# Optimization experiments

Measured on AMD Instinct MI355X. Metric: run time of the kernel, lower is better.

## Reference

```python
import jax, jax.numpy as jnp
import numpy as np

KS = (16, 16, 16)  # k per layer

def _knn_idx(pts, k):
    # pts: (P, C). Exclude self (knn_graph default loop=False).
    P = pts.shape[0]
    sq = jnp.sum(pts * pts, axis=1)
    d2 = sq[:, None] + sq[None, :] - 2.0 * (pts @ pts.T)  # (P, P)
    d2 = d2.at[jnp.arange(P), jnp.arange(P)].set(jnp.inf)
    _, idx = jax.lax.top_k(-d2, k)  # (P, k) nearest neighbors
    return idx

def _edge_conv(h, idx, W, b):
    # h: (P, C); idx: (P, k); W: (2C, Cout)
    hi = h[:, None, :]                      # (P, 1, C)
    hj = h[idx]                             # (P, k, C) gather
    msg = jnp.concatenate([jnp.broadcast_to(hi, hj.shape), hj - hi], axis=-1)
    m = msg @ W + b                         # (P, k, Cout)
    return jnp.max(m, axis=1)               # max aggregation -> (P, Cout)

def setup_inputs() -> dict:
    key = jax.random.key(0)
    ks = jax.random.split(key, 12)
    B, N, d = 2, 4096, 3
    chans = [d, 64, 128, 256]
    inp = {"x": jax.random.normal(ks[0], (B, N, d), dtype=jnp.float32)}
    for i in range(3):
        cin, cout = chans[i], chans[i + 1]
        s = 1.0 / np.sqrt(2 * cin)
        inp[f"W{i+1}"] = jax.random.uniform(ks[1 + 2 * i], (2 * cin, cout), jnp.float32, -s, s)
        inp[f"b{i+1}"] = jax.random.uniform(ks[2 + 2 * i], (cout,), jnp.float32, -s, s)
    s1 = 1.0 / np.sqrt(256.0)
    inp["fW1"] = jax.random.uniform(ks[7], (256, 128), jnp.float32, -s1, s1)
    inp["fb1"] = jax.random.uniform(ks[8], (128,), jnp.float32, -s1, s1)
    s2 = 1.0 / np.sqrt(128.0)
    inp["fW2"] = jax.random.uniform(ks[9], (128, 1), jnp.float32, -s2, s2)
    inp["fb2"] = jax.random.uniform(ks[10], (1,), jnp.float32, -s2, s2)
    return inp

def reference(x, W1, b1, W2, b2, W3, b3, fW1, fb1, fW2, fb2):
    B, N, _ = x.shape
    h = x.reshape(B * N, -1)  # KNN spans flattened batch (batch=None in source)
    for (W, b, k) in ((W1, b1, KS[0]), (W2, b2, KS[1]), (W3, b3, KS[2])):
        idx = _knn_idx(h, k)
        h = jax.nn.relu(_edge_conv(h, idx, W, b))
    out = jax.nn.relu(h @ fW1 + fb1) @ fW2 + fb2  # (P, 1)
    return out.reshape(B, N, 1)
```

## Files before the change

### kernel.cpp

```cpp
#include <hip/hip_runtime.h>
#include <hip/hip_bf16.h>

#define PTS 8192
#define NSPLIT 8

__device__ __forceinline__ void top_init(float (&bd)[16], int (&bi)[16]) {
#pragma unroll
  for (int t = 0; t < 16; ++t) { bd[t] = 3e38f; bi[t] = 0; }
}

__device__ __forceinline__ void top_insert(float (&bd)[16], int (&bi)[16], float d, int j) {
  if (d < bd[15]) {
#pragma unroll
    for (int t = 15; t >= 0; --t) {
      bool c  = d < bd[t];
      bool cp = (t > 0) ? (d < bd[t - 1]) : false;
      float nd = cp ? bd[t - 1] : d;
      int   ni = cp ? bi[t - 1] : j;
      if (c) { bd[t] = nd; bi[t] = ni; }
    }
  }
}

__global__ void sqnorm_kernel(const float* __restrict__ h, float* __restrict__ sq, int C) {
  int i = blockIdx.x * 256 + threadIdx.x;
  if (i >= PTS) return;
  const float* r = h + (size_t)i * C;
  float s = 0.f;
  if ((C & 3) == 0) {
    for (int k = 0; k < C; k += 4) {
      float4 v = *(const float4*)(r + k);
      s += v.x * v.x + v.y * v.y + v.z * v.z + v.w * v.w;
    }
  } else {
    for (int k = 0; k < C; ++k) s += r[k] * r[k];
  }
  sq[i] = s;
}

template <int C>
__global__ __launch_bounds__(256) void knn_kernel(const float* __restrict__ H,
                                                  const float* __restrict__ sq,
                                                  float* __restrict__ pd,
                                                  int* __restrict__ pi) {
  constexpr int KC = (C < 32) ? C : 32;
  constexpr int NC = C / KC;
  constexpr int TT = (PTS / NSPLIT) / 64;
  constexpr int N  = TT * NC;

  __shared__ __align__(128) float AsF[C * 64];
  __shared__ __align__(128) float S[2 * 32 * 64];

  const int tid  = threadIdx.x;
  const int b    = blockIdx.x;
  const int sy   = b & 7;
  const int sx   = b >> 3;
  const int row0 = sx * 64;
  const int cb   = sy * (PTS / NSPLIT);
  const int tx = tid & 15, ty = tid >> 4;
  const int r_ = tid & 63, g_ = tid >> 6;

  if constexpr (C >= 32) {
    const int r = tid >> 2, q = tid & 3;
#pragma unroll
    for (int j = 0; j < C / 16; ++j) {
      float4 v = *(const float4*)(H + (size_t)(row0 + r) * C + (q + j * 4) * 4);
      float vv[4] = {v.x, v.y, v.z, v.w};
#pragma unroll
      for (int e = 0; e < 4; ++e)
        AsF[((q + j * 4) * 4 + e) * 64 + r] = vv[e];
    }
  } else {
    if (tid < 16 * C) {
      float4 v = *(const float4*)(H + (size_t)row0 * C + tid * 4);
      float vv[4] = {v.x, v.y, v.z, v.w};
#pragma unroll
      for (int e = 0; e < 4; ++e) {
        int gi = tid * 4 + e;
        AsF[(gi % C) * 64 + gi / C] = vv[e];
      }
    }
  }

  float sqr[4];
#pragma unroll
  for (int u = 0; u < 4; ++u) sqr[u] = sq[row0 + ty * 4 + u];

  float bd[16]; int bi[16];
  top_init(bd, bi);

  float4 st0 = make_float4(0.f, 0.f, 0.f, 0.f);
  float4 st1 = make_float4(0.f, 0.f, 0.f, 0.f);
  auto stage_load = [&](int n1) {
    if constexpr (C >= 32) {
      const int c = tid >> 2, qj = tid & 3;
      const float* src = H + (size_t)(cb + (n1 / NC) * 64 + c) * C + (n1 % NC) * KC + qj * 8;
      st0 = *(const float4*)(src);
      st1 = *(const float4*)(src + 4);
    } else {
      if (tid < 16 * C) st0 = *(const float4*)(H + (size_t)(cb + n1 * 64) * C + tid * 4);
    }
  };
  auto stage_write = [&](int n1) {
    float* B = S + (n1 & 1) * 2048;
    if constexpr (C >= 32) {
      const int c = tid >> 2, qj = tid & 3;
      float v0[4] = {st0.x, st0.y, st0.z, st0.w};
      float v1[4] = {st1.x, st1.y, st1.z, st1.w};
#pragma unroll
      for (int e = 0; e < 4; ++e) {
        B[(qj * 8 + e) * 64 + c]     = v0[e];
        B[(qj * 8 + 4 + e) * 64 + c] = v1[e];
      }
    } else {
      if (tid < 16 * C) {
        float v0[4] = {st0.x, st0.y, st0.z, st0.w};
#pragma unroll
        for (int e = 0; e < 4; ++e) {
          int gi = tid * 4 + e;
          B[(gi % C) * 64 + gi / C] = v0[e];
        }
      }
    }
  };

  stage_load(0);
  stage_write(0);
  __syncthreads();

  float acc[4][4] = {};
  for (int n = 0; n < N; ++n) {
    if (n + 1 < N) stage_load(n + 1);
    const float* Bh = S + (n & 1) * 2048;
    const int kc = (n % NC) * KC;
#pragma unroll
    for (int k = 0; k < KC; ++k) {
      float4 a4 = *(const float4*)(AsF + (kc + k) * 64 + ty * 4);
      float4 b4 = *(const float4*)(Bh + k * 64 + tx * 4);
      float a[4]  = {a4.x, a4.y, a4.z, a4.w};
      float bb[4] = {b4.x, b4.y, b4.z, b4.w};
#pragma unroll
      for (int u = 0; u < 4; ++u)
#pragma unroll
        for (int v = 0; v < 4; ++v)
          acc[u][v] += a[u] * bb[v];
    }
    if ((n % NC) == NC - 1) {
      const int ct = (n / NC) * 64;
      float sqc[4];
#pragma unroll
      for (int v = 0; v < 4; ++v) sqc[v] = sq[cb + ct + tx * 4 + v];
      __syncthreads();
#pragma unroll
      for (int u = 0; u < 4; ++u) {
        int row = ty * 4 + u;
        int gr  = row0 + row;
        float dv[4];
#pragma unroll
        for (int v = 0; v < 4; ++v) {
          float d2 = sqr[u] + sqc[v] - 2.f * acc[u][v];
          if (gr == cb + ct + tx * 4 + v) d2 = 3e38f;
          dv[v] = d2;
          acc[u][v] = 0.f;
        }
        *(float4*)(S + row * 64 + ((tx * 4) ^ ((row & 7) << 2))) =
            make_float4(dv[0], dv[1], dv[2], dv[3]);
      }
      __syncthreads();
      const int cbase = cb + ct;
      const int swr = (r_ & 7) << 2;
      unsigned mask = 0;
#pragma unroll
      for (int q = 0; q < 16; ++q) {
        int cc = g_ * 16 + ((q + r_) & 15);
        float d = S[r_ * 64 + (cc ^ swr)];
        if (d < bd[15]) mask |= (1u << q);
      }
      while (__ballot(mask != 0)) {
        if (mask) {
          int q = __ffs(mask) - 1;
          mask &= mask - 1;
          int cc = g_ * 16 + ((q + r_) & 15);
          float d = S[r_ * 64 + (cc ^ swr)];
          top_insert(bd, bi, d, cbase + cc);
        }
      }
      __syncthreads();
    }
    if (n + 1 < N) {
      stage_write(n + 1);
      __syncthreads();
    }
  }

  if (g_ == 1 || g_ == 3) {
    float* base = S + (g_ == 3 ? 2048 : 0) + r_ * 32;
#pragma unroll
    for (int t = 0; t < 16; ++t) {
      int s = (t + r_) & 15;
      base[s] = bd[t];
      ((int*)base)[16 + s] = bi[t];
    }
  }
  __syncthreads();
  if (g_ == 0 || g_ == 2) {
    const float* base = S + (g_ == 2 ? 2048 : 0) + r_ * 32;
    for (int t = 0; t < 16; ++t) {
      int s = (t + r_) & 15;
      float d = base[s];
      if (d >= bd[15]) break;
      top_insert(bd, bi, d, ((const int*)base)[16 + s]);
    }
  }
  __syncthreads();
  if (g_ == 2) {
    float* base = S + r_ * 32;
#pragma unroll
    for (int t = 0; t < 16; ++t) {
      int s = (t + r_) & 15;
      base[s] = bd[t];
      ((int*)base)[16 + s] = bi[t];
    }
  }
  __syncthreads();
  if (g_ == 0) {
    const float* base = S + r_ * 32;
    for (int t = 0; t < 16; ++t) {
      int s = (t + r_) & 15;
      float d = base[s];
      if (d >= bd[15]) break;
      top_insert(bd, bi, d, ((const int*)base)[16 + s]);
    }
    size_t basep = ((size_t)(row0 + r_) * NSPLIT + sy) * 16;
#pragma unroll
    for (int t = 0; t < 16; ++t) { pd[basep + t] = bd[t]; pi[basep + t] = bi[t]; }
  }
}

__global__ void knn_merge_kernel(const float* __restrict__ pd, const int* __restrict__ pi,
                                 int* __restrict__ idx) {
  int i = blockIdx.x * 256 + threadIdx.x;
  if (i >= PTS) return;
  float bd[16]; int bi[16];
  top_init(bd, bi);
  const float* d  = pd + (size_t)i * (NSPLIT * 16);
  const int*   ii = pi + (size_t)i * (NSPLIT * 16);
  for (int L = 0; L < NSPLIT; ++L) {
    for (int t = 0; t < 16; ++t) {
      float dv = d[L * 16 + t];
      if (dv >= bd[15]) break;
      top_insert(bd, bi, dv, ii[L * 16 + t]);
    }
  }
#pragma unroll
  for (int t = 0; t < 16; ++t) idx[(size_t)i * 16 + t] = bi[t];
}

__global__ __launch_bounds__(256) void gemm_fg_kernel(const float* __restrict__ A,
                                                      const float* __restrict__ Wt,
                                                      const float* __restrict__ Wb,
                                                      const float* __restrict__ bias,
                                                      float* __restrict__ F, float* __restrict__ G,
                                                      int K, int N) {
  __shared__ float As[16][68];
  __shared__ float Bs[16][68];
  const int tid  = threadIdx.x;
  const int row0 = blockIdx.x * 64, col0 = blockIdx.y * 64;
  const float* B = (blockIdx.z == 0) ? Wt : Wb;
  float* O       = (blockIdx.z == 0) ? F  : G;
  const int tx = tid & 15, ty = tid >> 4;
  float acc[4][4] = {};
  for (int k0 = 0; k0 < K; k0 += 16) {
    __syncthreads();
#pragma unroll
    for (int l = 0; l < 4; ++l) {
      int rr = (tid >> 4) + l * 16, kk = tid & 15;
      As[kk][rr] = (k0 + kk < K) ? A[(size_t)(row0 + rr) * K + k0 + kk] : 0.f;
      int cc = tid & 63, k2 = (tid >> 6) + l * 4;
      Bs[k2][cc] = (k0 + k2 < K) ? B[(size_t)(k0 + k2) * N + col0 + cc] : 0.f;
    }
    __syncthreads();
#pragma unroll
    for (int k = 0; k < 16; ++k) {
      float4 a4 = *(const float4*)&As[k][ty * 4];
      float4 b4 = *(const float4*)&Bs[k][tx * 4];
      float a[4] = {a4.x, a4.y, a4.z, a4.w};
      float b[4] = {b4.x, b4.y, b4.z, b4.w};
#pragma unroll
      for (int u = 0; u < 4; ++u)
#pragma unroll
        for (int v = 0; v < 4; ++v)
          acc[u][v] += a[u] * b[v];
    }
  }
  float bv[4] = {0.f, 0.f, 0.f, 0.f};
  if (blockIdx.z == 0) {
#pragma unroll
    for (int v = 0; v < 4; ++v) bv[v] = bias[col0 + tx * 4 + v];
  }
#pragma unroll
  for (int u = 0; u < 4; ++u)
#pragma unroll
    for (int v = 0; v < 4; ++v)
      O[(size_t)(row0 + ty * 4 + u) * N + col0 + tx * 4 + v] = acc[u][v] + bv[v];
}

__global__ void gather_max_kernel(const float* __restrict__ F, const float* __restrict__ G,
                                  const int* __restrict__ idx, float* __restrict__ Ho, int Cn) {
  int t = blockIdx.x * 256 + threadIdx.x;
  int per = Cn >> 2;
  int i = t / per;
  if (i >= PTS) return;
  int c = (t - i * per) * 4;
  const int* ji = idx + (size_t)i * 16;
  float4 m = make_float4(-3e38f, -3e38f, -3e38f, -3e38f);
#pragma unroll
  for (int s = 0; s < 16; ++s) {
    float4 v = *(const float4*)(G + (size_t)ji[s] * Cn + c);
    m.x = fmaxf(m.x, v.x); m.y = fmaxf(m.y, v.y);
    m.z = fmaxf(m.z, v.z); m.w = fmaxf(m.w, v.w);
  }
  float4 gi = *(const float4*)(G + (size_t)i * Cn + c);
  float4 f  = *(const float4*)(F + (size_t)i * Cn + c);
  float4 o;
  o.x = fmaxf(f.x - gi.x + m.x, 0.f);
  o.y = fmaxf(f.y - gi.y + m.y, 0.f);
  o.z = fmaxf(f.z - gi.z + m.z, 0.f);
  o.w = fmaxf(f.w - gi.w + m.w, 0.f);
  *(float4*)(Ho + (size_t)i * Cn + c) = o;
}

__global__ __launch_bounds__(256) void mlp_kernel(const float* __restrict__ h3,
                                                  const float* __restrict__ fW1,
                                                  const float* __restrict__ fb1,
                                                  const float* __restrict__ fW2,
                                                  const float* __restrict__ fb2,
                                                  float* __restrict__ out) {
  __shared__ float hs[16][260];
  __shared__ float ws[64][128];
  __shared__ float red[4][8];
  const int tid = threadIdx.x;
  const int p0  = blockIdx.x * 16;
#pragma unroll
  for (int l = 0; l < 16; ++l) {
    int ii = l * 256 + tid;
    hs[ii >> 8][ii & 255] = h3[(size_t)(p0 + (ii >> 8)) * 256 + (ii & 255)];
  }
  const int c = tid & 127, half = tid >> 7;
  float acc[8];
#pragma unroll
  for (int pp = 0; pp < 8; ++pp) acc[pp] = fb1[c];
  for (int k0 = 0; k0 < 256; k0 += 64) {
    __syncthreads();
#pragma unroll
    for (int l = 0; l < 32; ++l) {
      int ii = l * 256 + tid;
      ws[ii >> 7][ii & 127] = fW1[(size_t)(k0 + (ii >> 7)) * 128 + (ii & 127)];
    }
    __syncthreads();
    for (int k = 0; k < 64; k += 4) {
      float w0 = ws[k][c], w1 = ws[k + 1][c], w2 = ws[k + 2][c], w3 = ws[k + 3][c];
#pragma unroll
      for (int pp = 0; pp < 8; ++pp) {
        float4 h4 = *(const float4*)&hs[half * 8 + pp][k0 + k];
        acc[pp] += h4.x * w0 + h4.y * w1 + h4.z * w2 + h4.w * w3;
      }
    }
  }
  float w2v = fW2[c];
  float s[8];
#pragma unroll
  for (int pp = 0; pp < 8; ++pp) s[pp] = fmaxf(acc[pp], 0.f) * w2v;
#pragma unroll
  for (int off = 32; off > 0; off >>= 1) {
#pragma unroll
    for (int pp = 0; pp < 8; ++pp) s[pp] += __shfl_down(s[pp], off);
  }
  if ((tid & 63) == 0) {
#pragma unroll
    for (int pp = 0; pp < 8; ++pp) red[tid >> 6][pp] = s[pp];
  }
  __syncthreads();
  if (tid < 16) {
    int hf = tid >> 3, pp = tid & 7;
    float v = red[hf * 2][pp] + red[hf * 2 + 1][pp] + fb2[0];
    out[p0 + hf * 8 + pp] = v;
  }
}

extern "C" void kernel_launch(void* const* d_in, const int* in_sizes, int n_in,
                              void* d_out, int out_size, void* d_ws, size_t ws_size,
                              hipStream_t stream) {
  (void)in_sizes; (void)n_in; (void)out_size; (void)ws_size;
  const float* x   = (const float*)d_in[0];
  const float* W1  = (const float*)d_in[1];
  const float* b1  = (const float*)d_in[2];
  const float* W2  = (const float*)d_in[3];
  const float* b2  = (const float*)d_in[4];
  const float* W3  = (const float*)d_in[5];
  const float* b3  = (const float*)d_in[6];
  const float* fW1 = (const float*)d_in[7];
  const float* fb1 = (const float*)d_in[8];
  const float* fW2 = (const float*)d_in[9];
  const float* fb2 = (const float*)d_in[10];

  float* w = (float*)d_ws;
  size_t o = 0;
  float* sq  = w + o; o += PTS;
  float* h1  = w + o; o += (size_t)PTS * 64;
  float* h2  = w + o; o += (size_t)PTS * 128;
  float* h3  = w + o; o += (size_t)PTS * 256;
  float* F   = w + o; o += (size_t)PTS * 256;
  float* G   = w + o; o += (size_t)PTS * 256;
  float* pd  = w + o; o += (size_t)PTS * 128;
  int*   pi  = (int*)(w + o); o += (size_t)PTS * 128;
  int*   idx = (int*)(w + o); o += (size_t)PTS * 16;

  const int KNN_GRID = (PTS / 64) * NSPLIT;

  sqnorm_kernel<<<PTS / 256, 256, 0, stream>>>(x, sq, 3);
  knn_kernel<3><<<KNN_GRID, 256, 0, stream>>>(x, sq, pd, pi);
  knn_merge_kernel<<<PTS / 256, 256, 0, stream>>>(pd, pi, idx);
  gemm_fg_kernel<<<dim3(PTS / 64, 1, 2), 256, 0, stream>>>(x, W1, W1 + 3 * 64, b1, F, G, 3, 64);
  gather_max_kernel<<<(PTS * 16 + 255) / 256, 256, 0, stream>>>(F, G, idx, h1, 64);

  sqnorm_kernel<<<PTS / 256, 256, 0, stream>>>(h1, sq, 64);
  knn_kernel<64><<<KNN_GRID, 256, 0, stream>>>(h1, sq, pd, pi);
  knn_merge_kernel<<<PTS / 256, 256, 0, stream>>>(pd, pi, idx);
  gemm_fg_kernel<<<dim3(PTS / 64, 2, 2), 256, 0, stream>>>(h1, W2, W2 + 64 * 128, b2, F, G, 64, 128);
  gather_max_kernel<<<(PTS * 32 + 255) / 256, 256, 0, stream>>>(F, G, idx, h2, 128);

  sqnorm_kernel<<<PTS / 256, 256, 0, stream>>>(h2, sq, 128);
  knn_kernel<128><<<KNN_GRID, 256, 0, stream>>>(h2, sq, pd, pi);
  knn_merge_kernel<<<PTS / 256, 256, 0, stream>>>(pd, pi, idx);
  gemm_fg_kernel<<<dim3(PTS / 64, 4, 2), 256, 0, stream>>>(h2, W3, W3 + 128 * 256, b3, F, G, 128, 256);
  gather_max_kernel<<<(PTS * 64 + 255) / 256, 256, 0, stream>>>(F, G, idx, h3, 256);

  mlp_kernel<<<PTS / 16, 256, 0, stream>>>(h3, fW1, fb1, fW2, fb2, (float*)d_out);
}
```

Measured before the change: 1.128 ms.

## Halve KNN row tile to 32 rows with 8-way column split per row

The KNN block now covers 32 query rows instead of 64, doubling the grid, and each thread computes a 2x4 accumulator tile. Candidate filtering gives each thread 8 columns per row, read as two float4 loads, and drops the ballot-synchronized insert loop. The final partial top-k merge starts with a shuffle-based merge between wave halves, then a single LDS merge of three partial lists. The goal is more parallelism and shorter per-thread insertion chains, at the cost of less A-tile reuse, more global B loads per point, and more partial lists to merge.

```diff
diff --git a/kernel.cpp b/kernel.cpp
--- a/kernel.cpp
+++ b/kernel.cpp
@@ -48,43 +48,46 @@
   constexpr int TT = (PTS / NSPLIT) / 64;
   constexpr int N  = TT * NC;
 
-  __shared__ __align__(128) float AsF[C * 64];
+  __shared__ __align__(128) float AsF[C * 32];
   __shared__ __align__(128) float S[2 * 32 * 64];
 
   const int tid  = threadIdx.x;
   const int b    = blockIdx.x;
   const int sy   = b & 7;
   const int sx   = b >> 3;
-  const int row0 = sx * 64;
+  const int row0 = sx * 32;
   const int cb   = sy * (PTS / NSPLIT);
   const int tx = tid & 15, ty = tid >> 4;
-  const int r_ = tid & 63, g_ = tid >> 6;
+  const int r_ = tid & 31;
+  const int g8 = tid >> 5;
+  const int l_ = tid & 63, w_ = tid >> 6;
 
   if constexpr (C >= 32) {
-    const int r = tid >> 2, q = tid & 3;
-#pragma unroll
-    for (int j = 0; j < C / 16; ++j) {
-      float4 v = *(const float4*)(H + (size_t)(row0 + r) * C + (q + j * 4) * 4);
+    const int r = tid >> 3, q0 = tid & 7;
+#pragma unroll
+    for (int j = 0; j < C / 32; ++j) {
+      int q = q0 + j * 8;
+      float4 v = *(const float4*)(H + (size_t)(row0 + r) * C + q * 4);
       float vv[4] = {v.x, v.y, v.z, v.w};
 #pragma unroll
       for (int e = 0; e < 4; ++e)
-        AsF[((q + j * 4) * 4 + e) * 64 + r] = vv[e];
+        AsF[(q * 4 + e) * 32 + r] = vv[e];
     }
   } else {
-    if (tid < 16 * C) {
+    if (tid < 8 * C) {
       float4 v = *(const float4*)(H + (size_t)row0 * C + tid * 4);
       float vv[4] = {v.x, v.y, v.z, v.w};
 #pragma unroll
       for (int e = 0; e < 4; ++e) {
         int gi = tid * 4 + e;
-        AsF[(gi % C) * 64 + gi / C] = vv[e];
-      }
-    }
-  }
-
-  float sqr[4];
-#pragma unroll
-  for (int u = 0; u < 4; ++u) sqr[u] = sq[row0 + ty * 4 + u];
+        AsF[(gi % C) * 32 + gi / C] = vv[e];
+      }
+    }
+  }
+
+  float sqr[2];
+#pragma unroll
+  for (int u = 0; u < 2; ++u) sqr[u] = sq[row0 + ty * 2 + u];
 
   float bd[16]; int bi[16];
   top_init(bd, bi);
@@ -128,19 +131,19 @@
   stage_write(0);
   __syncthreads();
 
-  float acc[4][4] = {};
+  float acc[2][4] = {};
   for (int n = 0; n < N; ++n) {
     if (n + 1 < N) stage_load(n + 1);
     const float* Bh = S + (n & 1) * 2048;
     const int kc = (n % NC) * KC;
 #pragma unroll
     for (int k = 0; k < KC; ++k) {
-      float4 a4 = *(const float4*)(AsF + (kc + k) * 64 + ty * 4);
+      float2 a2 = *(const float2*)(AsF + (kc + k) * 32 + ty * 2);
       float4 b4 = *(const float4*)(Bh + k * 64 + tx * 4);
-      float a[4]  = {a4.x, a4.y, a4.z, a4.w};
+      float a[2]  = {a2.x, a2.y};
       float bb[4] = {b4.x, b4.y, b4.z, b4.w};
 #pragma unroll
-      for (int u = 0; u < 4; ++u)
+      for (int u = 0; u < 2; ++u)
 #pragma unroll
         for (int v = 0; v < 4; ++v)
           acc[u][v] += a[u] * bb[v];
@@ -152,8 +155,8 @@
       for (int v = 0; v < 4; ++v) sqc[v] = sq[cb + ct + tx * 4 + v];
       __syncthreads();
 #pragma unroll
-      for (int u = 0; u < 4; ++u) {
-        int row = ty * 4 + u;
+      for (int u = 0; u < 2; ++u) {
+        int row = ty * 2 + u;
         int gr  = row0 + row;
         float dv[4];
 #pragma unroll
@@ -169,21 +172,23 @@
       __syncthreads();
       const int cbase = cb + ct;
       const int swr = (r_ & 7) << 2;
+      float4 f0 = *(const float4*)(S + r_ * 64 + ((g8 * 8) ^ swr));
+      float4 f1 = *(const float4*)(S + r_ * 64 + ((g8 * 8 + 4) ^ swr));
       unsigned mask = 0;
-#pragma unroll
-      for (int q = 0; q < 16; ++q) {
-        int cc = g_ * 16 + ((q + r_) & 15);
+      if (f0.x < bd[15]) mask |= 1u;
+      if (f0.y < bd[15]) mask |= 2u;
+      if (f0.z < bd[15]) mask |= 4u;
+      if (f0.w < bd[15]) mask |= 8u;
+      if (f1.x < bd[15]) mask |= 16u;
+      if (f1.y < bd[15]) mask |= 32u;
+      if (f1.z < bd[15]) mask |= 64u;
+      if (f1.w < bd[15]) mask |= 128u;
+      while (mask) {
+        int q = __ffs(mask) - 1;
+        mask &= mask - 1;
+        int cc = g8 * 8 + q;
         float d = S[r_ * 64 + (cc ^ swr)];
-        if (d < bd[15]) mask |= (1u << q);
-      }
-      while (__ballot(mask != 0)) {
-        if (mask) {
-          int q = __ffs(mask) - 1;
-          mask &= mask - 1;
-          int cc = g_ * 16 + ((q + r_) & 15);
-          float d = S[r_ * 64 + (cc ^ swr)];
-          top_insert(bd, bi, d, cbase + cc);
-        }
+        top_insert(bd, bi, d, cbase + cc);
       }
       __syncthreads();
     }
@@ -193,8 +198,16 @@
     }
   }
 
-  if (g_ == 1 || g_ == 3) {
-    float* base = S + (g_ == 3 ? 2048 : 0) + r_ * 32;
+  for (int t = 0; t < 16; ++t) {
+    float d = __shfl(bd[t], (l_ & 31) + 32);
+    int   i = __shfl(bi[t], (l_ & 31) + 32);
+    unsigned long long m = __ballot((l_ < 32) && (d < bd[15]));
+    if (!m) break;
+    if (l_ < 32) top_insert(bd, bi, d, i);
+  }
+  __syncthreads();
+  if (w_ > 0 && l_ < 32) {
+    float* base = S + (w_ - 1) * 1024 + r_ * 32;
 #pragma unroll
     for (int t = 0; t < 16; ++t) {
       int s = (t + r_) & 15;
@@ -203,33 +216,15 @@
     }
   }
   __syncthreads();
-  if (g_ == 0 || g_ == 2) {
-    const float* base = S + (g_ == 2 ? 2048 : 0) + r_ * 32;
-    for (int t = 0; t < 16; ++t) {
-      int s = (t + r_) & 15;
-      float d = base[s];
-      if (d >= bd[15]) break;
-      top_insert(bd, bi, d, ((const int*)base)[16 + s]);
-    }
-  }
-  __syncthreads();
-  if (g_ == 2) {
-    float* base = S + r_ * 32;
-#pragma unroll
-    for (int t = 0; t < 16; ++t) {
-      int s = (t + r_) & 15;
-      base[s] = bd[t];
-      ((int*)base)[16 + s] = bi[t];
-    }
-  }
-  __syncthreads();
-  if (g_ == 0) {
-    const float* base = S + r_ * 32;
-    for (int t = 0; t < 16; ++t) {
-      int s = (t + r_) & 15;
-      float d = base[s];
-      if (d >= bd[15]) break;
-      top_insert(bd, bi, d, ((const int*)base)[16 + s]);
+  if (w_ == 0 && l_ < 32) {
+    for (int L = 0; L < 3; ++L) {
+      const float* base = S + L * 1024 + r_ * 32;
+      for (int t = 0; t < 16; ++t) {
+        int s = (t + r_) & 15;
+        float d = base[s];
+        if (d >= bd[15]) break;
+        top_insert(bd, bi, d, ((const int*)base)[16 + s]);
+      }
     }
     size_t basep = ((size_t)(row0 + r_) * NSPLIT + sy) * 16;
 #pragma unroll
@@ -416,7 +411,7 @@
   int*   pi  = (int*)(w + o); o += (size_t)PTS * 128;
   int*   idx = (int*)(w + o); o += (size_t)PTS * 16;
 
-  const int KNN_GRID = (PTS / 64) * NSPLIT;
+  const int KNN_GRID = (PTS / 32) * NSPLIT;
 
   sqnorm_kernel<<<PTS / 256, 256, 0, stream>>>(x, sq, 3);
   knn_kernel<3><<<KNN_GRID, 256, 0, stream>>>(x, sq, pd, pi);
```

After: 1.219 ms. 1.08x slower.

## Halve kNN block to 128 threads with 8x4 register tiles and two-way selection

Applied to the files above, without the earlier changes.

Reworks the kNN kernel to run 128 threads per block, each computing an 8x4 tile of the distance block. Candidate selection is split across two 64-thread groups scanning 32 columns each with vectorized LDS reads, and the cross-group merge shrinks to a single step. The ballot-guarded insertion loop becomes a plain per-thread loop. This raises arithmetic per LDS load and cuts merge/sync overhead, but doubles per-thread top-k insertion work and reduces threads available per block.

```diff
diff --git a/kernel.cpp b/kernel.cpp
--- a/kernel.cpp
+++ b/kernel.cpp
@@ -39,7 +39,7 @@
 }
 
 template <int C>
-__global__ __launch_bounds__(256) void knn_kernel(const float* __restrict__ H,
+__global__ __launch_bounds__(128) void knn_kernel(const float* __restrict__ H,
                                                   const float* __restrict__ sq,
                                                   float* __restrict__ pd,
                                                   int* __restrict__ pi) {
@@ -61,14 +61,15 @@
   const int r_ = tid & 63, g_ = tid >> 6;
 
   if constexpr (C >= 32) {
-    const int r = tid >> 2, q = tid & 3;
-#pragma unroll
-    for (int j = 0; j < C / 16; ++j) {
-      float4 v = *(const float4*)(H + (size_t)(row0 + r) * C + (q + j * 4) * 4);
+    const int r = tid >> 1, h = tid & 1;
+#pragma unroll
+    for (int j = 0; j < C / 8; ++j) {
+      int q = h * (C / 8) + j;
+      float4 v = *(const float4*)(H + (size_t)(row0 + r) * C + q * 4);
       float vv[4] = {v.x, v.y, v.z, v.w};
 #pragma unroll
       for (int e = 0; e < 4; ++e)
-        AsF[((q + j * 4) * 4 + e) * 64 + r] = vv[e];
+        AsF[(q * 4 + e) * 64 + r] = vv[e];
     }
   } else {
     if (tid < 16 * C) {
@@ -82,43 +83,45 @@
     }
   }
 
-  float sqr[4];
-#pragma unroll
-  for (int u = 0; u < 4; ++u) sqr[u] = sq[row0 + ty * 4 + u];
+  float sqr[8];
+#pragma unroll
+  for (int u = 0; u < 8; ++u) sqr[u] = sq[row0 + ty * 8 + u];
 
   float bd[16]; int bi[16];
   top_init(bd, bi);
 
-  float4 st0 = make_float4(0.f, 0.f, 0.f, 0.f);
-  float4 st1 = make_float4(0.f, 0.f, 0.f, 0.f);
+  float4 st[4];
+#pragma unroll
+  for (int j = 0; j < 4; ++j) st[j] = make_float4(0.f, 0.f, 0.f, 0.f);
+
   auto stage_load = [&](int n1) {
     if constexpr (C >= 32) {
-      const int c = tid >> 2, qj = tid & 3;
-      const float* src = H + (size_t)(cb + (n1 / NC) * 64 + c) * C + (n1 % NC) * KC + qj * 8;
-      st0 = *(const float4*)(src);
-      st1 = *(const float4*)(src + 4);
+      const int c = tid & 63, kq = tid >> 6;
+      const float* src = H + (size_t)(cb + (n1 / NC) * 64 + c) * C + (n1 % NC) * KC + kq * 16;
+#pragma unroll
+      for (int j = 0; j < 4; ++j) st[j] = *(const float4*)(src + j * 4);
     } else {
-      if (tid < 16 * C) st0 = *(const float4*)(H + (size_t)(cb + n1 * 64) * C + tid * 4);
+      if (tid < 16 * C) st[0] = *(const float4*)(H + (size_t)(cb + n1 * 64) * C + tid * 4);
     }
   };
   auto stage_write = [&](int n1) {
     float* B = S + (n1 & 1) * 2048;
     if constexpr (C >= 32) {
-      const int c = tid >> 2, qj = tid & 3;
-      float v0[4] = {st0.x, st0.y, st0.z, st0.w};
-      float v1[4] = {st1.x, st1.y, st1.z, st1.w};
-#pragma unroll
-      for (int e = 0; e < 4; ++e) {
-        B[(qj * 8 + e) * 64 + c]     = v0[e];
-        B[(qj * 8 + 4 + e) * 64 + c] = v1[e];
+      const int c = tid & 63, kq = tid >> 6;
+#pragma unroll
+      for (int j = 0; j < 4; ++j) {
+        float vv[4] = {st[j].x, st[j].y, st[j].z, st[j].w};
+#pragma unroll
+        for (int e = 0; e < 4; ++e)
+          B[(kq * 16 + j * 4 + e) * 64 + c] = vv[e];
       }
     } else {
       if (tid < 16 * C) {
-        float v0[4] = {st0.x, st0.y, st0.z, st0.w};
+        float vv[4] = {st[0].x, st[0].y, st[0].z, st[0].w};
 #pragma unroll
         for (int e = 0; e < 4; ++e) {
           int gi = tid * 4 + e;
-          B[(gi % C) * 64 + gi / C] = v0[e];
+          B[(gi % C) * 64 + gi / C] = vv[e];
         }
       }
     }
@@ -128,62 +131,63 @@
   stage_write(0);
   __syncthreads();
 
-  float acc[4][4] = {};
+  float acc[8][4] = {};
   for (int n = 0; n < N; ++n) {
     if (n + 1 < N) stage_load(n + 1);
     const float* Bh = S + (n & 1) * 2048;
     const int kc = (n % NC) * KC;
 #pragma unroll
     for (int k = 0; k < KC; ++k) {
-      float4 a4 = *(const float4*)(AsF + (kc + k) * 64 + ty * 4);
-      float4 b4 = *(const float4*)(Bh + k * 64 + tx * 4);
-      float a[4]  = {a4.x, a4.y, a4.z, a4.w};
+      float4 a40 = *(const float4*)(AsF + (kc + k) * 64 + ty * 8);
+      float4 a41 = *(const float4*)(AsF + (kc + k) * 64 + ty * 8 + 4);
+      float4 b4  = *(const float4*)(Bh + k * 64 + tx * 4);
+      float a[8]  = {a40.x, a40.y, a40.z, a40.w, a41.x, a41.y, a41.z, a41.w};
       float bb[4] = {b4.x, b4.y, b4.z, b4.w};
 #pragma unroll
-      for (int u = 0; u < 4; ++u)
+      for (int u = 0; u < 8; ++u)
 #pragma unroll
         for (int v = 0; v < 4; ++v)
           acc[u][v] += a[u] * bb[v];
     }
     if ((n % NC) == NC - 1) {
       const int ct = (n / NC) * 64;
+      const int cbase = cb + ct;
       float sqc[4];
 #pragma unroll
-      for (int v = 0; v < 4; ++v) sqc[v] = sq[cb + ct + tx * 4 + v];
+      for (int v = 0; v < 4; ++v) sqc[v] = sq[cbase + tx * 4 + v];
       __syncthreads();
 #pragma unroll
-      for (int u = 0; u < 4; ++u) {
-        int row = ty * 4 + u;
+      for (int u = 0; u < 8; ++u) {
+        int row = ty * 8 + u;
         int gr  = row0 + row;
+        int sw  = (row & 7) << 2;
         float dv[4];
 #pragma unroll
         for (int v = 0; v < 4; ++v) {
           float d2 = sqr[u] + sqc[v] - 2.f * acc[u][v];
-          if (gr == cb + ct + tx * 4 + v) d2 = 3e38f;
+          if (gr == cbase + tx * 4 + v) d2 = 3e38f;
           dv[v] = d2;
           acc[u][v] = 0.f;
         }
-        *(float4*)(S + row * 64 + ((tx * 4) ^ ((row & 7) << 2))) =
-            make_float4(dv[0], dv[1], dv[2], dv[3]);
+        *(float4*)(S + row * 64 + ((tx * 4) ^ sw)) = make_float4(dv[0], dv[1], dv[2], dv[3]);
       }
       __syncthreads();
-      const int cbase = cb + ct;
       const int swr = (r_ & 7) << 2;
       unsigned mask = 0;
 #pragma unroll
-      for (int q = 0; q < 16; ++q) {
-        int cc = g_ * 16 + ((q + r_) & 15);
+      for (int j = 0; j < 8; ++j) {
+        float4 f = *(const float4*)(S + r_ * 64 + ((g_ * 32 + j * 4) ^ swr));
+        if (f.x < bd[15]) mask |= (1u << (j * 4 + 0));
+        if (f.y < bd[15]) mask |= (1u << (j * 4 + 1));
+        if (f.z < bd[15]) mask |= (1u << (j * 4 + 2));
+        if (f.w < bd[15]) mask |= (1u << (j * 4 + 3));
+      }
+      while (mask) {
+        int q = __ffs(mask) - 1;
+        mask &= mask - 1;
+        int cc = g_ * 32 + q;
         float d = S[r_ * 64 + (cc ^ swr)];
-        if (d < bd[15]) mask |= (1u << q);
-      }
-      while (__ballot(mask != 0)) {
-        if (mask) {
-          int q = __ffs(mask) - 1;
-          mask &= mask - 1;
-          int cc = g_ * 16 + ((q + r_) & 15);
-          float d = S[r_ * 64 + (cc ^ swr)];
-          top_insert(bd, bi, d, cbase + cc);
-        }
+        top_insert(bd, bi, d, cbase + cc);
       }
       __syncthreads();
     }
@@ -193,27 +197,8 @@
     }
   }
 
-  if (g_ == 1 || g_ == 3) {
-    float* base = S + (g_ == 3 ? 2048 : 0) + r_ * 32;
-#pragma unroll
-    for (int t = 0; t < 16; ++t) {
-      int s = (t + r_) & 15;
-      base[s] = bd[t];
-      ((int*)base)[16 + s] = bi[t];
-    }
-  }
   __syncthreads();
-  if (g_ == 0 || g_ == 2) {
-    const float* base = S + (g_ == 2 ? 2048 : 0) + r_ * 32;
-    for (int t = 0; t < 16; ++t) {
-      int s = (t + r_) & 15;
-      float d = base[s];
-      if (d >= bd[15]) break;
-      top_insert(bd, bi, d, ((const int*)base)[16 + s]);
-    }
-  }
-  __syncthreads();
-  if (g_ == 2) {
+  if (g_ == 1) {
     float* base = S + r_ * 32;
 #pragma unroll
     for (int t = 0; t < 16; ++t) {
@@ -419,19 +404,19 @@
   const int KNN_GRID = (PTS / 64) * NSPLIT;
 
   sqnorm_kernel<<<PTS / 256, 256, 0, stream>>>(x, sq, 3);
-  knn_kernel<3><<<KNN_GRID, 256, 0, stream>>>(x, sq, pd, pi);
+  knn_kernel<3><<<KNN_GRID, 128, 0, stream>>>(x, sq, pd, pi);
   knn_merge_kernel<<<PTS / 256, 256, 0, stream>>>(pd, pi, idx);
   gemm_fg_kernel<<<dim3(PTS / 64, 1, 2), 256, 0, stream>>>(x, W1, W1 + 3 * 64, b1, F, G, 3, 64);
   gather_max_kernel<<<(PTS * 16 + 255) / 256, 256, 0, stream>>>(F, G, idx, h1, 64);
 
   sqnorm_kernel<<<PTS / 256, 256, 0, stream>>>(h1, sq, 64);
-  knn_kernel<64><<<KNN_GRID, 256, 0, stream>>>(h1, sq, pd, pi);
+  knn_kernel<64><<<KNN_GRID, 128, 0, stream>>>(h1, sq, pd, pi);
   knn_merge_kernel<<<PTS / 256, 256, 0, stream>>>(pd, pi, idx);
   gemm_fg_kernel<<<dim3(PTS / 64, 2, 2), 256, 0, stream>>>(h1, W2, W2 + 64 * 128, b2, F, G, 64, 128);
   gather_max_kernel<<<(PTS * 32 + 255) / 256, 256, 0, stream>>>(F, G, idx, h2, 128);
 
   sqnorm_kernel<<<PTS / 256, 256, 0, stream>>>(h2, sq, 128);
-  knn_kernel<128><<<KNN_GRID, 256, 0, stream>>>(h2, sq, pd, pi);
+  knn_kernel<128><<<KNN_GRID, 128, 0, stream>>>(h2, sq, pd, pi);
   knn_merge_kernel<<<PTS / 256, 256, 0, stream>>>(pd, pi, idx);
   gemm_fg_kernel<<<dim3(PTS / 64, 4, 2), 256, 0, stream>>>(h2, W3, W3 + 128 * 256, b3, F, G, 128, 256);
   gather_max_kernel<<<(PTS * 64 + 255) / 256, 256, 0, stream>>>(F, G, idx, h3, 256);
```

Result: faster. 1.022 ms (-9.3%).

## Widen KNN column tile to 128 points with 4x8 register blocking

Applied to the files above, without the earlier changes.

Doubles the candidate column tile in the KNN kernel from 64 to 128 points, so each thread now computes a 4x8 block of distances and the shared staging buffer doubles in size. Staging loads are reorganized (16 floats per thread for C>=32, scalar xyz loads for C=3), and top-k candidate scanning uses float4 shared reads plus a plain per-thread loop instead of a ballot-driven loop. This halves the number of tile iterations and barriers per block and raises arithmetic per shared load, at the cost of more registers and LDS, which may reduce occupancy.

```diff
diff --git a/kernel.cpp b/kernel.cpp
--- a/kernel.cpp
+++ b/kernel.cpp
@@ -45,11 +45,11 @@
                                                   int* __restrict__ pi) {
   constexpr int KC = (C < 32) ? C : 32;
   constexpr int NC = C / KC;
-  constexpr int TT = (PTS / NSPLIT) / 64;
+  constexpr int TT = (PTS / NSPLIT) / 128;
   constexpr int N  = TT * NC;
 
   __shared__ __align__(128) float AsF[C * 64];
-  __shared__ __align__(128) float S[2 * 32 * 64];
+  __shared__ __align__(128) float S[2 * 32 * 128];
 
   const int tid  = threadIdx.x;
   const int b    = blockIdx.x;
@@ -61,14 +61,15 @@
   const int r_ = tid & 63, g_ = tid >> 6;
 
   if constexpr (C >= 32) {
-    const int r = tid >> 2, q = tid & 3;
+    const int r = tid & 63, h = tid >> 6;
 #pragma unroll
     for (int j = 0; j < C / 16; ++j) {
-      float4 v = *(const float4*)(H + (size_t)(row0 + r) * C + (q + j * 4) * 4);
+      int q = h * (C / 16) + j;
+      float4 v = *(const float4*)(H + (size_t)(row0 + r) * C + q * 4);
       float vv[4] = {v.x, v.y, v.z, v.w};
 #pragma unroll
       for (int e = 0; e < 4; ++e)
-        AsF[((q + j * 4) * 4 + e) * 64 + r] = vv[e];
+        AsF[(q * 4 + e) * 64 + r] = vv[e];
     }
   } else {
     if (tid < 16 * C) {
@@ -89,37 +90,39 @@
   float bd[16]; int bi[16];
   top_init(bd, bi);
 
-  float4 st0 = make_float4(0.f, 0.f, 0.f, 0.f);
-  float4 st1 = make_float4(0.f, 0.f, 0.f, 0.f);
+  float4 st[4];
+#pragma unroll
+  for (int j = 0; j < 4; ++j) st[j] = make_float4(0.f, 0.f, 0.f, 0.f);
+
   auto stage_load = [&](int n1) {
     if constexpr (C >= 32) {
-      const int c = tid >> 2, qj = tid & 3;
-      const float* src = H + (size_t)(cb + (n1 / NC) * 64 + c) * C + (n1 % NC) * KC + qj * 8;
-      st0 = *(const float4*)(src);
-      st1 = *(const float4*)(src + 4);
+      const int c = tid & 127, kq = tid >> 7;
+      const float* src = H + (size_t)(cb + (n1 / NC) * 128 + c) * C + (n1 % NC) * KC + kq * 16;
+#pragma unroll
+      for (int j = 0; j < 4; ++j) st[j] = *(const float4*)(src + j * 4);
     } else {
-      if (tid < 16 * C) st0 = *(const float4*)(H + (size_t)(cb + n1 * 64) * C + tid * 4);
+      if (tid < 128) {
+        const float* src = H + (size_t)(cb + n1 * 128 + tid) * C;
+        st[0].x = src[0]; st[0].y = src[1]; st[0].z = src[2];
+      }
     }
   };
   auto stage_write = [&](int n1) {
-    float* B = S + (n1 & 1) * 2048;
+    float* B = S + (n1 & 1) * 4096;
     if constexpr (C >= 32) {
-      const int c = tid >> 2, qj = tid & 3;
-      float v0[4] = {st0.x, st0.y, st0.z, st0.w};
-      float v1[4] = {st1.x, st1.y, st1.z, st1.w};
-#pragma unroll
-      for (int e = 0; e < 4; ++e) {
-        B[(qj * 8 + e) * 64 + c]     = v0[e];
-        B[(qj * 8 + 4 + e) * 64 + c] = v1[e];
+      const int c = tid & 127, kq = tid >> 7;
+#pragma unroll
+      for (int j = 0; j < 4; ++j) {
+        float vv[4] = {st[j].x, st[j].y, st[j].z, st[j].w};
+#pragma unroll
+        for (int e = 0; e < 4; ++e)
+          B[(kq * 16 + j * 4 + e) * 128 + c] = vv[e];
       }
     } else {
-      if (tid < 16 * C) {
-        float v0[4] = {st0.x, st0.y, st0.z, st0.w};
-#pragma unroll
-        for (int e = 0; e < 4; ++e) {
-          int gi = tid * 4 + e;
-          B[(gi % C) * 64 + gi / C] = v0[e];
-        }
+      if (tid < 128) {
+        B[0 * 128 + tid] = st[0].x;
+        B[1 * 128 + tid] = st[0].y;
+        B[2 * 128 + tid] = st[0].z;
       }
     }
   };
@@ -128,62 +131,75 @@
   stage_write(0);
   __syncthreads();
 
-  float acc[4][4] = {};
+  float acc[4][8] = {};
   for (int n = 0; n < N; ++n) {
     if (n + 1 < N) stage_load(n + 1);
-    const float* Bh = S + (n & 1) * 2048;
+    const float* Bh = S + (n & 1) * 4096;
     const int kc = (n % NC) * KC;
 #pragma unroll
     for (int k = 0; k < KC; ++k) {
-      float4 a4 = *(const float4*)(AsF + (kc + k) * 64 + ty * 4);
-      float4 b4 = *(const float4*)(Bh + k * 64 + tx * 4);
+      float4 a4  = *(const float4*)(AsF + (kc + k) * 64 + ty * 4);
+      float4 b40 = *(const float4*)(Bh + k * 128 + tx * 4);
+      float4 b41 = *(const float4*)(Bh + k * 128 + 64 + tx * 4);
       float a[4]  = {a4.x, a4.y, a4.z, a4.w};
-      float bb[4] = {b4.x, b4.y, b4.z, b4.w};
+      float bb[8] = {b40.x, b40.y, b40.z, b40.w, b41.x, b41.y, b41.z, b41.w};
 #pragma unroll
       for (int u = 0; u < 4; ++u)
 #pragma unroll
-        for (int v = 0; v < 4; ++v)
+        for (int v = 0; v < 8; ++v)
           acc[u][v] += a[u] * bb[v];
     }
     if ((n % NC) == NC - 1) {
-      const int ct = (n / NC) * 64;
-      float sqc[4];
-#pragma unroll
-      for (int v = 0; v < 4; ++v) sqc[v] = sq[cb + ct + tx * 4 + v];
+      const int ct = (n / NC) * 128;
+      const int cbase = cb + ct;
+      float sqc[8];
+#pragma unroll
+      for (int v = 0; v < 4; ++v) {
+        sqc[v]     = sq[cbase + tx * 4 + v];
+        sqc[v + 4] = sq[cbase + 64 + tx * 4 + v];
+      }
       __syncthreads();
 #pragma unroll
       for (int u = 0; u < 4; ++u) {
         int row = ty * 4 + u;
         int gr  = row0 + row;
-        float dv[4];
+        int sw  = (row & 7) << 2;
+        float dv[8];
 #pragma unroll
         for (int v = 0; v < 4; ++v) {
           float d2 = sqr[u] + sqc[v] - 2.f * acc[u][v];
-          if (gr == cb + ct + tx * 4 + v) d2 = 3e38f;
+          if (gr == cbase + tx * 4 + v) d2 = 3e38f;
           dv[v] = d2;
           acc[u][v] = 0.f;
+          float d2h = sqr[u] + sqc[v + 4] - 2.f * acc[u][v + 4];
+          d2h += 0.f;
+          if (gr == cbase + 64 + tx * 4 + v) d2h = 3e38f;
+          dv[v + 4] = d2h;
+          acc[u][v + 4] = 0.f;
         }
-        *(float4*)(S + row * 64 + ((tx * 4) ^ ((row & 7) << 2))) =
-            make_float4(dv[0], dv[1], dv[2], dv[3]);
+        *(float4*)(S + row * 128 + ((tx * 4) ^ sw)) = make_float4(dv[0], dv[1], dv[2], dv[3]);
+        *(float4*)(S + row * 128 + 64 + ((tx * 4) ^ sw)) = make_float4(dv[4], dv[5], dv[6], dv[7]);
       }
       __syncthreads();
-      const int cbase = cb + ct;
       const int swr = (r_ & 7) << 2;
       unsigned mask = 0;
 #pragma unroll
-      for (int q = 0; q < 16; ++q) {
-        int cc = g_ * 16 + ((q + r_) & 15);
-        float d = S[r_ * 64 + (cc ^ swr)];
-        if (d < bd[15]) mask |= (1u << q);
-      }
-      while (__ballot(mask != 0)) {
-        if (mask) {
-          int q = __ffs(mask) - 1;
-          mask &= mask - 1;
-          int cc = g_ * 16 + ((q + r_) & 15);
-          float d = S[r_ * 64 + (cc ^ swr)];
-          top_insert(bd, bi, d, cbase + cc);
-        }
+      for (int j = 0; j < 8; ++j) {
+        int c0 = g_ * 32 + j * 4;
+        int off = (c0 & 64) + ((c0 & 63) ^ swr);
+        float4 f = *(const float4*)(S + r_ * 128 + off);
+        if (f.x < bd[15]) mask |= (1u << (j * 4 + 0));
+        if (f.y < bd[15]) mask |= (1u << (j * 4 + 1));
+        if (f.z < bd[15]) mask |= (1u << (j * 4 + 2));
+        if (f.w < bd[15]) mask |= (1u << (j * 4 + 3));
+      }
+      while (mask) {
+        int q = __ffs(mask) - 1;
+        mask &= mask - 1;
+        int cc = g_ * 32 + q;
+        int off = (cc & 64) + ((cc & 63) ^ swr);
+        float d = S[r_ * 128 + off];
+        top_insert(bd, bi, d, cbase + cc);
       }
       __syncthreads();
     }
@@ -193,6 +209,7 @@
     }
   }
 
+  __syncthreads();
   if (g_ == 1 || g_ == 3) {
     float* base = S + (g_ == 3 ? 2048 : 0) + r_ * 32;
 #pragma unroll
```

Result: slower. 1.338 ms (+18.7%).
